# Performance work log

Measured on AMD Instinct MI355X. Metric: run time of the kernel, lower is better.

The kernel has to match this reference:

```python
import jax, jax.numpy as jnp
import numpy as np
import math

B = 8192
N_MODELS = 64
T_PER_SPLIT = 16
MAXLEAF = 64
EMB = 32
BN_EPS = 1e-5


def setup_inputs() -> dict:
    key = jax.random.key(0)
    k1, k2, k3 = jax.random.split(key, 3)
    # leaf indices per (sample, model*tree), values in [0, maxleaf)
    x = jax.random.randint(k1, (B, N_MODELS * T_PER_SPLIT), 0, MAXLEAF, dtype=jnp.int32)
    # embed_w ~ N(0, sqrt(1/max_ntree_per_split))
    embed_w = jax.random.normal(k2, (N_MODELS, T_PER_SPLIT * MAXLEAF, EMB), dtype=jnp.float32) * math.sqrt(1.0 / T_PER_SPLIT)
    # BatchNorm1d affine params (gamma=1, beta=0 at init)
    bn_gamma = jnp.ones((N_MODELS * EMB,), dtype=jnp.float32)
    bn_beta = jnp.zeros((N_MODELS * EMB,), dtype=jnp.float32)
    # BatchDense(n_models, embsize, 1): weight (M, E, 1) squeezed to (M, E), bias zeros (M,)
    stdv = math.sqrt(6.0 / (EMB + 1))
    bout_w = jax.random.uniform(k3, (N_MODELS, EMB), dtype=jnp.float32, minval=-stdv, maxval=stdv)
    bout_b = jnp.zeros((N_MODELS,), dtype=jnp.float32)
    return {"x": x, "embed_w": embed_w, "bn_gamma": bn_gamma, "bn_beta": bn_beta,
            "bout_w": bout_w, "bout_b": bout_b}


def reference(x, embed_w, bn_gamma, bn_beta, bout_w, bout_b):
    # x: (B, M*T) int leaf indices; embed_w: (M, T*L, E)
    Bn = x.shape[0]
    M, TL, E = embed_w.shape
    T = x.shape[1] // M
    L = TL // T
    # one_hot + bmm == per-tree gather from embed_w, summed over trees
    idx = x.reshape(Bn, M, T) + jnp.arange(T, dtype=x.dtype) * L  # (B, M, T) into TL axis
    emb = embed_w[jnp.arange(M)[None, :, None], idx]              # (B, M, T, E) gather
    h = emb.sum(axis=2).reshape(Bn, M * E)                        # (B, M*E)
    # BatchNorm1d (training-mode batch statistics, biased variance as in torch)
    mean = h.mean(axis=0)
    var = h.var(axis=0)
    h = (h - mean) / jnp.sqrt(var + BN_EPS) * bn_gamma + bn_beta
    # dropout is identity in eval mode
    h = h.reshape(Bn, M, E)
    # BatchDense: per-model linear E -> 1
    out = jnp.einsum('bme,me->bm', h, bout_w) + bout_b            # (B, M)
    sum_out = out.sum(axis=-1, keepdims=True)                     # (B, 1)
    return (sum_out, out)
```

## Files before the change

### kernel.cpp

```cpp
#include <hip/hip_runtime.h>

constexpr int B_TOT = 8192;
constexpr int NM    = 64;
constexpr int TT    = 16;
constexpr int LF    = 64;
constexpr int EM    = 32;
constexpr int XROW  = NM * TT;
constexpr int TROWS = TT * LF;

__device__ __forceinline__ unsigned bf2(float lo, float hi) {
    unsigned ul = __float_as_uint(lo), uh = __float_as_uint(hi);
    ul += 0x7fffu + ((ul >> 16) & 1u);
    uh += 0x7fffu + ((uh >> 16) & 1u);
    return (ul >> 16) | (uh & 0xffff0000u);
}

__device__ __forceinline__ void accum8(float* h, const uint4 v) {
    h[0] += __uint_as_float(v.x << 16);
    h[1] += __uint_as_float(v.x & 0xffff0000u);
    h[2] += __uint_as_float(v.y << 16);
    h[3] += __uint_as_float(v.y & 0xffff0000u);
    h[4] += __uint_as_float(v.z << 16);
    h[5] += __uint_as_float(v.z & 0xffff0000u);
    h[6] += __uint_as_float(v.w << 16);
    h[7] += __uint_as_float(v.w & 0xffff0000u);
}

__global__ __launch_bounds__(512, 4) void k_stats_lds(
    const int* __restrict__ x, const float* __restrict__ tbl,
    float* __restrict__ wsum, float* __restrict__ wsumsq)
{
    __shared__ uint4 tb[TROWS * 4];
    __shared__ int   xb[128 * 16];
    __shared__ float red[2][8][32];

    const int m     = blockIdx.x & 63;
    const int chunk = blockIdx.x >> 6;
    const int tid   = threadIdx.x;
    const int f     = tid & 3;
    const int grp   = tid >> 2;
    const int b0    = chunk * 1024;

    {
        const float4* __restrict__ src = (const float4*)(tbl + (size_t)m * (TROWS * EM));
#pragma unroll
        for (int i = 0; i < 8; ++i) {
            const int o = tid + i * 512;
            const float4 a = src[o * 2];
            const float4 c = src[o * 2 + 1];
            uint4 p;
            p.x = bf2(a.x, a.y); p.y = bf2(a.z, a.w);
            p.z = bf2(c.x, c.y); p.w = bf2(c.z, c.w);
            tb[o] = p;
        }
    }

    const int4* __restrict__ xg = (const int4*)(x + (size_t)(b0 + grp) * XROW + m * TT);
    int4 xr = xg[f];

    float s[8], s2[8];
#pragma unroll
    for (int k = 0; k < 8; ++k) { s[k] = 0.f; s2[k] = 0.f; }

    for (int p = 0; p < 8; ++p) {
        __syncthreads();
        ((int4*)xb)[grp * 4 + f] = xr;
        if (p < 7) {
            const int4* nxt = (const int4*)(x + (size_t)(b0 + (p + 1) * 128 + grp) * XROW + m * TT);
            xr = nxt[f];
        }
        __syncthreads();

        float h[8];
#pragma unroll
        for (int k = 0; k < 8; ++k) h[k] = 0.f;

#pragma unroll
        for (int tq = 0; tq < 4; ++tq) {
            const int4 q = ((const int4*)xb)[grp * 4 + tq];
            const int rbase = tq * 256;
            accum8(h, tb[(q.x + rbase      ) * 4 + f]);
            accum8(h, tb[(q.y + rbase +  64) * 4 + f]);
            accum8(h, tb[(q.z + rbase + 128) * 4 + f]);
            accum8(h, tb[(q.w + rbase + 192) * 4 + f]);
        }
#pragma unroll
        for (int k = 0; k < 8; ++k) { s[k] += h[k]; s2[k] = fmaf(h[k], h[k], s2[k]); }
    }

#pragma unroll
    for (int off = 4; off <= 32; off <<= 1) {
#pragma unroll
        for (int k = 0; k < 8; ++k) {
            s[k]  += __shfl_xor(s[k],  off);
            s2[k] += __shfl_xor(s2[k], off);
        }
    }
    const int wave = tid >> 6;
    if ((tid & 63) < 4) {
#pragma unroll
        for (int k = 0; k < 8; ++k) {
            red[0][wave][f * 8 + k] = s[k];
            red[1][wave][f * 8 + k] = s2[k];
        }
    }
    __syncthreads();
    if (tid < 32) {
        float a = 0.f, a2 = 0.f;
#pragma unroll
        for (int w = 0; w < 8; ++w) { a += red[0][w][tid]; a2 += red[1][w][tid]; }
        atomicAdd(&wsum[m * EM + tid], a);
        atomicAdd(&wsumsq[m * EM + tid], a2);
    }
}

__global__ __launch_bounds__(256) void k_prep(
    const float* __restrict__ tbl,
    const float* __restrict__ gamma, const float* __restrict__ beta,
    const float* __restrict__ bw, const float* __restrict__ bb,
    const float* __restrict__ wsum, const float* __restrict__ wsumsq,
    float* __restrict__ Cm, float* __restrict__ g2)
{
    const int m    = blockIdx.x >> 2;
    const int part = blockIdx.x & 3;
    __shared__ float a_s[EM];
    if (threadIdx.x < EM) {
        const int e  = threadIdx.x;
        const int ch = m * EM + e;
        const float inv_n = 1.f / (float)B_TOT;
        const float mean = wsum[ch] * inv_n;
        const float var  = wsumsq[ch] * inv_n - mean * mean;
        const float istd = rsqrtf(var + 1e-5f);
        const float g = gamma[ch];
        const float w = bw[ch];
        a_s[e] = istd * g * w;
        float ct = (beta[ch] - mean * istd * g) * w;
#pragma unroll
        for (int off = 16; off > 0; off >>= 1) ct += __shfl_down(ct, off, 32);
        if (e == 0 && part == 0) Cm[m] = bb[m] + ct;
    }
    __syncthreads();

    const float* __restrict__ tblm = tbl + (size_t)m * (TROWS * EM);
    const int row = part * 256 + threadIdx.x;
    const float4* rp = (const float4*)(tblm + row * EM);
    float acc = 0.f;
#pragma unroll
    for (int i = 0; i < 8; ++i) {
        const float4 v = rp[i];
        acc += v.x * a_s[i*4+0] + v.y * a_s[i*4+1]
             + v.z * a_s[i*4+2] + v.w * a_s[i*4+3];
    }
    g2[row * NM + m] = acc;
}

__global__ __launch_bounds__(1024, 8) void k_out(
    const int* __restrict__ x, const float* __restrict__ g2,
    const float* __restrict__ Cm, float* __restrict__ out)
{
    __shared__ float slab[4 * LF * NM];
    const int tid  = threadIdx.x;
    const int wid  = tid >> 6;
    const int lane = tid & 63;
    const int b    = blockIdx.x * 16 + wid;

    const int4* xp = (const int4*)(x + (size_t)b * XROW + lane * TT);
    const int4 q0 = xp[0], q1 = xp[1], q2 = xp[2], q3 = xp[3];
    const int idxs[16] = {q0.x,q0.y,q0.z,q0.w, q1.x,q1.y,q1.z,q1.w,
                          q2.x,q2.y,q2.z,q2.w, q3.x,q3.y,q3.z,q3.w};

    float acc = 0.f;
#pragma unroll
    for (int ph = 0; ph < 4; ++ph) {
        if (ph) __syncthreads();
        const float4* src = (const float4*)(g2 + (size_t)ph * (4 * LF * NM));
        float4* dst = (float4*)slab;
#pragma unroll
        for (int j = 0; j < 4; ++j) dst[tid + j * 1024] = src[tid + j * 1024];
        __syncthreads();
#pragma unroll
        for (int tt = 0; tt < 4; ++tt)
            acc += slab[tt * (LF * NM) + idxs[ph * 4 + tt] * NM + lane];
    }

    const float o = acc + Cm[lane];
    float s = o;
#pragma unroll
    for (int off = 32; off > 0; off >>= 1) s += __shfl_down(s, off);
    out[B_TOT + (size_t)b * NM + lane] = o;
    if (lane == 0) out[b] = s;
}

extern "C" void kernel_launch(void* const* d_in, const int* in_sizes, int n_in,
                              void* d_out, int out_size, void* d_ws, size_t ws_size,
                              hipStream_t stream) {
    const int*   x       = (const int*)d_in[0];
    const float* embed_w = (const float*)d_in[1];
    const float* gamma   = (const float*)d_in[2];
    const float* beta    = (const float*)d_in[3];
    const float* bout_w  = (const float*)d_in[4];
    const float* bout_b  = (const float*)d_in[5];
    float* out = (float*)d_out;

    float* ws     = (float*)d_ws;
    float* wsum   = ws;
    float* wsumsq = ws + 2048;
    float* Cm     = ws + 4096;
    float* g2     = ws + 4160;

    (void)hipMemsetAsync(wsum, 0, 4096 * sizeof(float), stream);

    k_stats_lds<<<dim3(512), dim3(512), 0, stream>>>(x, embed_w, wsum, wsumsq);
    k_prep<<<dim3(256), dim3(256),  0, stream>>>(embed_w, gamma, beta, bout_w,
                                                 bout_b, wsum, wsumsq, Cm, g2);
    k_out <<<dim3(512), dim3(1024), 0, stream>>>(x, g2, Cm, out);
}
```

Before: 116.0 us.

## Store stats table as fp16 and accumulate with packed half2 adds

The stats kernel now converts the embedding table to fp16 in LDS instead of bf16 and sums the 16 tree embeddings with packed half2 adds rather than unpacking each value to fp32. Each thread also loads its whole 16-index x row directly into registers and prefetches the next one, which removes the LDS staging of indices and the two barriers per iteration. The aim is fewer ALU instructions and less synchronisation in the gather loop. The cost is fp16 accumulation error in the batch statistics and redundant global loads of x, since four threads now each read the full row.

```diff
diff --git a/kernel.cpp b/kernel.cpp
--- a/kernel.cpp
+++ b/kernel.cpp
@@ -1,4 +1,5 @@
 #include <hip/hip_runtime.h>
+#include <hip/hip_fp16.h>
 
 constexpr int B_TOT = 8192;
 constexpr int NM    = 64;
@@ -8,30 +9,11 @@
 constexpr int XROW  = NM * TT;
 constexpr int TROWS = TT * LF;
 
-__device__ __forceinline__ unsigned bf2(float lo, float hi) {
-    unsigned ul = __float_as_uint(lo), uh = __float_as_uint(hi);
-    ul += 0x7fffu + ((ul >> 16) & 1u);
-    uh += 0x7fffu + ((uh >> 16) & 1u);
-    return (ul >> 16) | (uh & 0xffff0000u);
-}
-
-__device__ __forceinline__ void accum8(float* h, const uint4 v) {
-    h[0] += __uint_as_float(v.x << 16);
-    h[1] += __uint_as_float(v.x & 0xffff0000u);
-    h[2] += __uint_as_float(v.y << 16);
-    h[3] += __uint_as_float(v.y & 0xffff0000u);
-    h[4] += __uint_as_float(v.z << 16);
-    h[5] += __uint_as_float(v.z & 0xffff0000u);
-    h[6] += __uint_as_float(v.w << 16);
-    h[7] += __uint_as_float(v.w & 0xffff0000u);
-}
-
-__global__ __launch_bounds__(512, 4) void k_stats_lds(
+__global__ __launch_bounds__(512, 4) void k_stats_f16(
     const int* __restrict__ x, const float* __restrict__ tbl,
     float* __restrict__ wsum, float* __restrict__ wsumsq)
 {
     __shared__ uint4 tb[TROWS * 4];
-    __shared__ int   xb[128 * 16];
     __shared__ float red[2][8][32];
 
     const int m     = blockIdx.x & 63;
@@ -49,43 +31,63 @@
             const float4 a = src[o * 2];
             const float4 c = src[o * 2 + 1];
             uint4 p;
-            p.x = bf2(a.x, a.y); p.y = bf2(a.z, a.w);
-            p.z = bf2(c.x, c.y); p.w = bf2(c.z, c.w);
+            __half2 h0 = __floats2half2_rn(a.x, a.y);
+            __half2 h1 = __floats2half2_rn(a.z, a.w);
+            __half2 h2 = __floats2half2_rn(c.x, c.y);
+            __half2 h3 = __floats2half2_rn(c.z, c.w);
+            p.x = *(unsigned*)&h0; p.y = *(unsigned*)&h1;
+            p.z = *(unsigned*)&h2; p.w = *(unsigned*)&h3;
             tb[o] = p;
         }
     }
 
-    const int4* __restrict__ xg = (const int4*)(x + (size_t)(b0 + grp) * XROW + m * TT);
-    int4 xr = xg[f];
+    const int4* xp = (const int4*)(x + (size_t)(b0 + grp) * XROW + m * TT);
+    int4 xa = xp[0], xb_ = xp[1], xc = xp[2], xd = xp[3];
 
     float s[8], s2[8];
 #pragma unroll
     for (int k = 0; k < 8; ++k) { s[k] = 0.f; s2[k] = 0.f; }
 
+    __syncthreads();
+
     for (int p = 0; p < 8; ++p) {
-        __syncthreads();
-        ((int4*)xb)[grp * 4 + f] = xr;
+        int4 na, nb, nc, nd;
         if (p < 7) {
-            const int4* nxt = (const int4*)(x + (size_t)(b0 + (p + 1) * 128 + grp) * XROW + m * TT);
-            xr = nxt[f];
-        }
-        __syncthreads();
-
-        float h[8];
-#pragma unroll
-        for (int k = 0; k < 8; ++k) h[k] = 0.f;
+            const int4* np = (const int4*)(x + (size_t)(b0 + (p + 1) * 128 + grp) * XROW + m * TT);
+            na = np[0]; nb = np[1]; nc = np[2]; nd = np[3];
+        }
+
+        __half2 h[4];
+#pragma unroll
+        for (int k = 0; k < 4; ++k) h[k] = __half2(__half(0.f), __half(0.f));
 
 #pragma unroll
         for (int tq = 0; tq < 4; ++tq) {
-            const int4 q = ((const int4*)xb)[grp * 4 + tq];
+            const int4 q = (tq == 0) ? xa : (tq == 1) ? xb_ : (tq == 2) ? xc : xd;
             const int rbase = tq * 256;
-            accum8(h, tb[(q.x + rbase      ) * 4 + f]);
-            accum8(h, tb[(q.y + rbase +  64) * 4 + f]);
-            accum8(h, tb[(q.z + rbase + 128) * 4 + f]);
-            accum8(h, tb[(q.w + rbase + 192) * 4 + f]);
-        }
-#pragma unroll
-        for (int k = 0; k < 8; ++k) { s[k] += h[k]; s2[k] = fmaf(h[k], h[k], s2[k]); }
+            const uint4 v0 = tb[(q.x + rbase      ) * 4 + f];
+            const uint4 v1 = tb[(q.y + rbase +  64) * 4 + f];
+            const uint4 v2 = tb[(q.z + rbase + 128) * 4 + f];
+            const uint4 v3 = tb[(q.w + rbase + 192) * 4 + f];
+            h[0] = __hadd2(h[0], __hadd2(__hadd2(*(const __half2*)&v0.x, *(const __half2*)&v1.x),
+                                         __hadd2(*(const __half2*)&v2.x, *(const __half2*)&v3.x)));
+            h[1] = __hadd2(h[1], __hadd2(__hadd2(*(const __half2*)&v0.y, *(const __half2*)&v1.y),
+                                         __hadd2(*(const __half2*)&v2.y, *(const __half2*)&v3.y)));
+            h[2] = __hadd2(h[2], __hadd2(__hadd2(*(const __half2*)&v0.z, *(const __half2*)&v1.z),
+                                         __hadd2(*(const __half2*)&v2.z, *(const __half2*)&v3.z)));
+            h[3] = __hadd2(h[3], __hadd2(__hadd2(*(const __half2*)&v0.w, *(const __half2*)&v1.w),
+                                         __hadd2(*(const __half2*)&v2.w, *(const __half2*)&v3.w)));
+        }
+
+#pragma unroll
+        for (int k = 0; k < 4; ++k) {
+            const float lo = __low2float(h[k]);
+            const float hi = __high2float(h[k]);
+            s[2*k]   += lo;  s2[2*k]   = fmaf(lo, lo, s2[2*k]);
+            s[2*k+1] += hi;  s2[2*k+1] = fmaf(hi, hi, s2[2*k+1]);
+        }
+
+        xa = na; xb_ = nb; xc = nc; xd = nd;
     }
 
 #pragma unroll
@@ -210,7 +212,7 @@
 
     (void)hipMemsetAsync(wsum, 0, 4096 * sizeof(float), stream);
 
-    k_stats_lds<<<dim3(512), dim3(512), 0, stream>>>(x, embed_w, wsum, wsumsq);
+    k_stats_f16<<<dim3(512), dim3(512), 0, stream>>>(x, embed_w, wsum, wsumsq);
     k_prep<<<dim3(256), dim3(256),  0, stream>>>(embed_w, gamma, beta, bout_w,
                                                  bout_b, wsum, wsumsq, Cm, g2);
     k_out <<<dim3(512), dim3(1024), 0, stream>>>(x, g2, Cm, out);
```

After: 111.4 us. -4.0%, faster.
